# Optimization experiments

Hardware: AMD Instinct MI355X
Metric: run time of the kernel (lower is better)

Reference implementation:

```python
import jax, jax.numpy as jnp
import numpy as np

WIN = 7
SHIFT = 3
HEADS = 12
DIM = 384
HID = 4 * DIM
B, H, W = 32, 56, 56
N = WIN * WIN  # window area
EPS = 1e-5


def _rel_pos_index():
    coords = np.stack(np.meshgrid(np.arange(WIN), np.arange(WIN), indexing='ij'))  # (2,7,7)
    flat = coords.reshape(2, -1)  # (2,49)
    rel = flat[:, :, None] - flat[:, None, :]  # (2,49,49)
    rel = rel.transpose(1, 2, 0)
    rel[:, :, 0] += WIN - 1
    rel[:, :, 1] += WIN - 1
    rel[:, :, 0] *= 2 * WIN - 1
    return rel.sum(-1)  # (49,49) indices into (2*7-1)^2=169 table


def _attn_mask():
    img = np.zeros((H, W), dtype=np.float32)
    hs = [(0, H - WIN), (H - WIN, H - SHIFT), (H - SHIFT, H)]
    ws = [(0, W - WIN), (W - WIN, W - SHIFT), (W - SHIFT, W)]
    cnt = 0
    for h0, h1 in hs:
        for w0, w1 in ws:
            img[h0:h1, w0:w1] = cnt
            cnt += 1
    mw = img.reshape(H // WIN, WIN, W // WIN, WIN).transpose(0, 2, 1, 3).reshape(-1, N)  # (nW,49)
    d = mw[:, None, :] - mw[:, :, None]
    return np.where(d != 0, -100.0, 0.0).astype(np.float32)  # (nW,49,49)


_RPI = jnp.asarray(_rel_pos_index())
_MASK = jnp.asarray(_attn_mask())


def _ln(t, w, b):
    m = t.mean(-1, keepdims=True)
    v = ((t - m) ** 2).mean(-1, keepdims=True)
    return (t - m) * jax.lax.rsqrt(v + EPS) * w + b


def setup_inputs() -> dict:
    key = jax.random.key(0)
    ks = jax.random.split(key, 16)
    s = 0.02
    return {
        'x': jax.random.normal(ks[0], (B, H, W, DIM), jnp.float32),
        'norm1_w': jnp.ones((DIM,), jnp.float32),
        'norm1_b': jnp.zeros((DIM,), jnp.float32),
        'qkv_w': jax.random.normal(ks[1], (3 * DIM, DIM), jnp.float32) * s,
        'qkv_b': jnp.zeros((3 * DIM,), jnp.float32),
        'rel_bias_table': jax.random.normal(ks[2], ((2 * WIN - 1) ** 2, HEADS), jnp.float32) * s,
        'proj_w': jax.random.normal(ks[3], (DIM, DIM), jnp.float32) * s,
        'proj_b': jnp.zeros((DIM,), jnp.float32),
        'norm2_w': jnp.ones((DIM,), jnp.float32),
        'norm2_b': jnp.zeros((DIM,), jnp.float32),
        'fc1_w': jax.random.normal(ks[4], (HID, DIM), jnp.float32) * s,
        'fc1_b': jnp.zeros((HID,), jnp.float32),
        'fc2_w': jax.random.normal(ks[5], (DIM, HID), jnp.float32) * s,
        'fc2_b': jnp.zeros((DIM,), jnp.float32),
    }


def reference(x, norm1_w, norm1_b, qkv_w, qkv_b, rel_bias_table, proj_w, proj_b,
              norm2_w, norm2_b, fc1_w, fc1_b, fc2_w, fc2_b):
    Bt, Ht, Wt, C = x.shape
    hd = C // HEADS
    nh, nw = Ht // WIN, Wt // WIN
    nWtot = nh * nw

    # ---- attention branch ----
    h = _ln(x, norm1_w, norm1_b)
    h = jnp.roll(h, (-SHIFT, -SHIFT), axis=(1, 2))
    # window partition -> (B*nW, N, C)
    hw = h.reshape(Bt, nh, WIN, nw, WIN, C).transpose(0, 1, 3, 2, 4, 5).reshape(-1, N, C)
    qkv = hw @ qkv_w.T + qkv_b  # (B_, N, 3C)
    qkv = qkv.reshape(-1, N, 3, HEADS, hd).transpose(2, 0, 3, 1, 4)
    q, k, v = qkv[0], qkv[1], qkv[2]  # (B_, heads, N, hd)
    scale = hd ** -0.5
    attn = jnp.einsum('bhnd,bhmd->bhnm', q * scale, k)
    bias = rel_bias_table[_RPI].transpose(2, 0, 1)  # (heads, N, N)
    attn = attn + bias[None]
    attn = attn.reshape(Bt, nWtot, HEADS, N, N) + _MASK[None, :, None]
    attn = jax.nn.softmax(attn, axis=-1).reshape(-1, HEADS, N, N)
    o = jnp.einsum('bhnm,bhmd->bhnd', attn, v)
    o = o.transpose(0, 2, 1, 3).reshape(-1, N, C)
    o = o @ proj_w.T + proj_b
    # window reverse + roll back
    o = o.reshape(Bt, nh, nw, WIN, WIN, C).transpose(0, 1, 3, 2, 4, 5).reshape(Bt, Ht, Wt, C)
    o = jnp.roll(o, (SHIFT, SHIFT), axis=(1, 2))
    x = x + o

    # ---- MLP branch ----
    h = _ln(x, norm2_w, norm2_b)
    h = jax.nn.gelu(h @ fc1_w.T + fc1_b, approximate=False)
    h = h @ fc2_w.T + fc2_b
    return x + h
```

## Files before the change

### kernel.cpp

```cpp
#include <hip/hip_runtime.h>
#include <hip/hip_bf16.h>
#include <math.h>

using bf16 = __hip_bfloat16;
typedef short bf16x8 __attribute__((ext_vector_type(8)));
typedef float f32x4 __attribute__((ext_vector_type(4)));

static constexpr int  TOK     = 100352;
static constexpr long QKV_SEG = 38535168L;

__device__ __forceinline__ float bf2f(short u) {
    return __uint_as_float(((unsigned)(unsigned short)u) << 16);
}
__device__ __forceinline__ short f2bs(float x) {
    union { bf16 b; short s; } u; u.b = __float2bfloat16(x); return u.s;
}
__device__ __forceinline__ void gload16(const void* g, void* l) {
    __builtin_amdgcn_global_load_lds(
        (const __attribute__((address_space(1))) unsigned int*)g,
        (__attribute__((address_space(3))) unsigned int*)l, 16, 0, 0);
}
__device__ __forceinline__ float gelu_fast(float x) {
    const float x2 = x * x;
    const float t1 = x * x2;
    const float y  = fmaf(0.071354816222f, t1, 1.5957691216f * x);
    const float e  = __expf(-y);
    return x * __frcp_rn(1.f + e);
}

__global__ __launch_bounds__(256)
void convert_w_kernel(const float* __restrict__ qkv_w, const float* __restrict__ proj_w,
                      const float* __restrict__ fc1_w, const float* __restrict__ fc2_w,
                      bf16* __restrict__ out)
{
    const int i4 = (blockIdx.x * 256 + threadIdx.x) * 4;
    if (i4 >= 1769472) return;
    const float* src; int off;
    if (i4 < 442368)       { src = qkv_w;  off = i4; }
    else if (i4 < 589824)  { src = proj_w; off = i4 - 442368; }
    else if (i4 < 1179648) { src = fc1_w;  off = i4 - 589824; }
    else                   { src = fc2_w;  off = i4 - 1179648; }
    const float4 v = *(const float4*)&src[off];
    out[i4+0] = __float2bfloat16(v.x);
    out[i4+1] = __float2bfloat16(v.y);
    out[i4+2] = __float2bfloat16(v.z);
    out[i4+3] = __float2bfloat16(v.w);
}

template<bool WINDOWED>
__global__ __launch_bounds__(256)
void ln_kernel(const float* __restrict__ x, const float* __restrict__ gw,
               const float* __restrict__ gb, bf16* __restrict__ out)
{
    const int wave = threadIdx.x >> 6;
    const int lane = threadIdx.x & 63;
    const long t = (long)blockIdx.x * 4 + wave;
    size_t src;
    if (WINDOWED) {
        int bb = (int)(t / 3136); int rem = (int)(t - (long)bb * 3136);
        int wIdx = rem / 49;      int n = rem - wIdx * 49;
        int wh = wIdx >> 3, ww = wIdx & 7;
        int yi = n / 7,     xi = n - yi * 7;
        int r = wh * 7 + yi + 3; if (r >= 56) r -= 56;
        int c = ww * 7 + xi + 3; if (c >= 56) c -= 56;
        src = ((size_t)bb * 3136 + (size_t)r * 56 + c) * 384;
    } else {
        src = (size_t)t * 384;
    }
    float v[6]; float s = 0.f, sq = 0.f;
    #pragma unroll
    for (int kk = 0; kk < 6; ++kk) {
        v[kk] = x[src + lane + 64 * kk];
        s += v[kk]; sq += v[kk] * v[kk];
    }
    #pragma unroll
    for (int o = 32; o > 0; o >>= 1) { s += __shfl_xor(s, o); sq += __shfl_xor(sq, o); }
    const float m   = s * (1.f / 384.f);
    const float var = sq * (1.f / 384.f) - m * m;
    const float rs  = rsqrtf(var + 1e-5f);
    #pragma unroll
    for (int kk = 0; kk < 6; ++kk) {
        int ch = lane + 64 * kk;
        out[(size_t)t * 384 + ch] = __float2bfloat16((v[kk] - m) * rs * gw[ch] + gb[ch]);
    }
}

template<int MODE>
__global__ __launch_bounds__(256)
void gemm_bt(const bf16* __restrict__ A, const bf16* __restrict__ W,
             const float* __restrict__ bias, bf16* __restrict__ outb,
             float* __restrict__ outf, const float* __restrict__ resid,
             int K, int tilesN)
{
    __shared__ bf16 As[128 * 64];
    __shared__ bf16 Bs[128 * 64];
    const int nwg = gridDim.x;
    const int b0  = blockIdx.x;
    const int swz = (b0 & 7) * (nwg >> 3) + (b0 >> 3);
    const int tm = swz / tilesN;
    const int tn = swz - tm * tilesN;
    const int tid  = threadIdx.x;
    const int lane = tid & 63;
    const int wid  = tid >> 6;
    const int wr = (wid >> 1) * 64;
    const int wc = (wid & 1) * 64;
    const int sr = tid >> 3;
    const int sc = (tid & 7) * 8;

    f32x4 acc[4][4];
    #pragma unroll
    for (int i = 0; i < 4; ++i)
        #pragma unroll
        for (int j = 0; j < 4; ++j) acc[i][j] = (f32x4)0.0f;

    const long am0 = (long)tm * 128;
    const int  bn0 = tn * 128;

    for (int k0 = 0; k0 < K; k0 += 64) {
        #pragma unroll
        for (int p = 0; p < 4; ++p) {
            const int row = p * 32 + sr;
            gload16(&A[(size_t)(am0 + row) * K + k0 + sc], &As[row * 64 + sc]);
            gload16(&W[(size_t)(bn0 + row) * K + k0 + sc], &Bs[row * 64 + sc]);
        }
        __syncthreads();
        #pragma unroll
        for (int kk = 0; kk < 2; ++kk) {
            const int kof = kk * 32 + (lane >> 4) * 8;
            bf16x8 aF[4], bF[4];
            #pragma unroll
            for (int mi = 0; mi < 4; ++mi)
                aF[mi] = *(const bf16x8*)&As[(wr + mi * 16 + (lane & 15)) * 64 + kof];
            #pragma unroll
            for (int ni = 0; ni < 4; ++ni)
                bF[ni] = *(const bf16x8*)&Bs[(wc + ni * 16 + (lane & 15)) * 64 + kof];
            #pragma unroll
            for (int ni = 0; ni < 4; ++ni)
                #pragma unroll
                for (int mi = 0; mi < 4; ++mi)
                    acc[ni][mi] = __builtin_amdgcn_mfma_f32_16x16x32_bf16(
                        bF[ni], aF[mi], acc[ni][mi], 0, 0, 0);
        }
        __syncthreads();
    }

    #pragma unroll
    for (int nf = 0; nf < 4; ++nf) {
        const int gn0 = bn0 + wc + nf * 16 + ((lane >> 4) << 2);
        const float4 bv = *(const float4*)&bias[gn0];
        int s3 = 0, hh = 0, d0 = 0;
        if (MODE == 0) {
            s3 = gn0 / 384; const int rem = gn0 - s3 * 384;
            hh = rem >> 5; d0 = rem & 31;
        }
        #pragma unroll
        for (int mf = 0; mf < 4; ++mf) {
            const long gm = am0 + wr + mf * 16 + (lane & 15);
            float vals[4];
            #pragma unroll
            for (int r = 0; r < 4; ++r) vals[r] = acc[nf][mf][r] + ((const float*)&bv)[r];

            if (MODE == 0) {
                long wwi = gm / 49; int ntok = (int)(gm - wwi * 49);
                size_t dst = (size_t)s3 * QKV_SEG
                           + ((size_t)(wwi * 12 + hh) * 49 + ntok) * 32 + d0;
                union { short h4[4]; uint2 u2; } pk;
                if (s3 == 0) {
                    #pragma unroll
                    for (int r = 0; r < 4; ++r)
                        pk.h4[r] = f2bs(vals[r] * 0.17677669529663687f);
                } else {
                    #pragma unroll
                    for (int r = 0; r < 4; ++r) pk.h4[r] = f2bs(vals[r]);
                }
                *(uint2*)&outb[dst] = pk.u2;
            } else if (MODE == 1) {
                int bb = (int)(gm / 3136); int rem = (int)(gm - (long)bb * 3136);
                int wIdx = rem / 49; int n = rem - wIdx * 49;
                int wh = wIdx >> 3, ww2 = wIdx & 7;
                int yi = n / 7,     xi = n - yi * 7;
                int rr = wh * 7 + yi + 3; if (rr >= 56) rr -= 56;
                int cc = ww2 * 7 + xi + 3; if (cc >= 56) cc -= 56;
                size_t dst = ((size_t)bb * 3136 + (size_t)rr * 56 + cc) * 384 + gn0;
                const float4 rv = *(const float4*)&resid[dst];
                float4 ov;
                ov.x = rv.x + vals[0]; ov.y = rv.y + vals[1];
                ov.z = rv.z + vals[2]; ov.w = rv.w + vals[3];
                *(float4*)&outf[dst] = ov;
            } else if (MODE == 2) {
                union { short h4[4]; uint2 u2; } pk;
                #pragma unroll
                for (int r = 0; r < 4; ++r) pk.h4[r] = f2bs(gelu_fast(vals[r]));
                *(uint2*)&outb[(size_t)gm * 1536 + gn0] = pk.u2;
            } else {
                size_t dst = (size_t)gm * 384 + gn0;
                const float4 rv = *(const float4*)&resid[dst];
                float4 ov;
                ov.x = rv.x + vals[0]; ov.y = rv.y + vals[1];
                ov.z = rv.z + vals[2]; ov.w = rv.w + vals[3];
                *(float4*)&outf[dst] = ov;
            }
        }
    }
}

__global__ __launch_bounds__(256)
void attn_mfma(const bf16* __restrict__ q, const bf16* __restrict__ k,
               const bf16* __restrict__ v, const float* __restrict__ table,
               bf16* __restrict__ o)
{
    __shared__ bf16  vt_s[4][2048];
    __shared__ bf16  p_s[4][4096];
    __shared__ float tbl_s[4][169];

    const int tid  = threadIdx.x;
    const int wid  = tid >> 6;
    const int lane = tid & 63;
    const int li = lane & 15, g = lane >> 4;
    const int gwh = blockIdx.x * 4 + wid;
    const int w = gwh / 12, h = gwh - w * 12;
    const int wIdx = w & 63;
    const int bh = wIdx >> 3, bw = wIdx & 7;
    const size_t base = (size_t)gwh * 1568;

    char* vt = (char*)vt_s[wid];
    char* ps = (char*)p_s[wid];

    for (int t = lane; t < 169; t += 64) tbl_s[wid][t] = table[t * 12 + h];

    {
        const int4 z = {0, 0, 0, 0};
        #pragma unroll
        for (int t = 0; t < 4; ++t) ((int4*)vt)[t * 64 + lane] = z;
        for (int t = lane; t < 196; t += 64) {
            const int j = t >> 2, d0 = (t & 3) * 8;
            bf16x8 row = *(const bf16x8*)&v[base + (size_t)j * 32 + d0];
            #pragma unroll
            for (int u = 0; u < 8; ++u) {
                const int d = d0 + u;
                int off = (d << 7) + (j << 1);
                off ^= (d & 7) << 4;
                *(short*)(vt + off) = row[u];
            }
        }
    }

    bf16x8 aK[4], bQ[4];
    const int koff = g * 8;
    #pragma unroll
    for (int mj = 0; mj < 4; ++mj)
        aK[mj] = *(const bf16x8*)&k[base + (size_t)(mj * 16 + li) * 32 + koff];
    #pragma unroll
    for (int ni = 0; ni < 4; ++ni)
        bQ[ni] = *(const bf16x8*)&q[base + (size_t)(ni * 16 + li) * 32 + koff];

    f32x4 acc[4][4];
    #pragma unroll
    for (int i = 0; i < 4; ++i)
        #pragma unroll
        for (int j = 0; j < 4; ++j) acc[i][j] = (f32x4)0.0f;
    #pragma unroll
    for (int mj = 0; mj < 4; ++mj)
        #pragma unroll
        for (int ni = 0; ni < 4; ++ni)
            acc[mj][ni] = __builtin_amdgcn_mfma_f32_16x16x32_bf16(
                aK[mj], bQ[ni], acc[mj][ni], 0, 0, 0);

    const bool bndH = (bh == 7), bndW = (bw == 7);
    #pragma unroll
    for (int ni = 0; ni < 4; ++ni) {
        const int i = ni * 16 + li;
        const int yi = i / 7, xi = i - yi * 7;
        const int ri = (bndH ? (yi < 4 ? 3 : 6) : 0) + (bndW ? (xi < 4 ? 1 : 2) : 0);
        float mx = -1e30f;
        #pragma unroll
        for (int mj = 0; mj < 4; ++mj)
            #pragma unroll
            for (int r = 0; r < 4; ++r) {
                const int j = mj * 16 + g * 4 + r;
                const int yj = j / 7, xj = j - yj * 7;
                int ridx = (yi - yj + 6) * 13 + (xi - xj + 6);
                ridx = max(0, min(168, ridx));
                float val = acc[mj][ni][r] + tbl_s[wid][ridx];
                const int rj = (bndH ? (yj < 4 ? 3 : 6) : 0) + (bndW ? (xj < 4 ? 1 : 2) : 0);
                if (ri != rj) val -= 100.f;
                if (j >= 49) val = -1e30f;
                acc[mj][ni][r] = val;
                mx = fmaxf(mx, val);
            }
        mx = fmaxf(mx, __shfl_xor(mx, 16));
        mx = fmaxf(mx, __shfl_xor(mx, 32));
        float sum = 0.f;
        #pragma unroll
        for (int mj = 0; mj < 4; ++mj)
            #pragma unroll
            for (int r = 0; r < 4; ++r) {
                const float p = __expf(acc[mj][ni][r] - mx);
                acc[mj][ni][r] = p; sum += p;
            }
        sum += __shfl_xor(sum, 16);
        sum += __shfl_xor(sum, 32);
        const float inv = 1.f / sum;
        #pragma unroll
        for (int mj = 0; mj < 4; ++mj) {
            union { short h4[4]; uint2 u2; } pk;
            #pragma unroll
            for (int r = 0; r < 4; ++r) pk.h4[r] = f2bs(acc[mj][ni][r] * inv);
            int off = (i << 7) + ((mj * 16 + g * 4) << 1);
            off ^= (i & 7) << 4;
            *(uint2*)(ps + off) = pk.u2;
        }
    }

    f32x4 acc2[2][4];
    #pragma unroll
    for (int i = 0; i < 2; ++i)
        #pragma unroll
        for (int j = 0; j < 4; ++j) acc2[i][j] = (f32x4)0.0f;
    #pragma unroll
    for (int kk = 0; kk < 2; ++kk) {
        bf16x8 aV[2], bP[4];
        #pragma unroll
        for (int md = 0; md < 2; ++md) {
            const int d = md * 16 + li;
            int off = (d << 7) + kk * 64 + g * 16;
            off ^= (d & 7) << 4;
            aV[md] = *(const bf16x8*)(vt + off);
        }
        #pragma unroll
        for (int ni = 0; ni < 4; ++ni) {
            const int i = ni * 16 + li;
            int off = (i << 7) + kk * 64 + g * 16;
            off ^= (i & 7) << 4;
            bP[ni] = *(const bf16x8*)(ps + off);
        }
        #pragma unroll
        for (int md = 0; md < 2; ++md)
            #pragma unroll
            for (int ni = 0; ni < 4; ++ni)
                acc2[md][ni] = __builtin_amdgcn_mfma_f32_16x16x32_bf16(
                    aV[md], bP[ni], acc2[md][ni], 0, 0, 0);
    }

    const size_t obase = (size_t)w * 49 * 384 + h * 32;
    #pragma unroll
    for (int ni = 0; ni < 4; ++ni) {
        const int i = ni * 16 + li;
        if (i < 49) {
            #pragma unroll
            for (int md = 0; md < 2; ++md) {
                const int d0 = md * 16 + g * 4;
                union { short h4[4]; uint2 u2; } pk;
                #pragma unroll
                for (int r = 0; r < 4; ++r) pk.h4[r] = f2bs(acc2[md][ni][r]);
                *(uint2*)&o[obase + (size_t)i * 384 + d0] = pk.u2;
            }
        }
    }
}

extern "C" void kernel_launch(void* const* d_in, const int* in_sizes, int n_in,
                              void* d_out, int out_size, void* d_ws, size_t ws_size,
                              hipStream_t stream) {
    const float* x      = (const float*)d_in[0];
    const float* n1w    = (const float*)d_in[1];
    const float* n1b    = (const float*)d_in[2];
    const float* qkv_w  = (const float*)d_in[3];
    const float* qkv_b  = (const float*)d_in[4];
    const float* table  = (const float*)d_in[5];
    const float* proj_w = (const float*)d_in[6];
    const float* proj_b = (const float*)d_in[7];
    const float* n2w    = (const float*)d_in[8];
    const float* n2b    = (const float*)d_in[9];
    const float* fc1_w  = (const float*)d_in[10];
    const float* fc1_b  = (const float*)d_in[11];
    const float* fc2_w  = (const float*)d_in[12];
    const float* fc2_b  = (const float*)d_in[13];
    float* out = (float*)d_out;

    char* ws = (char*)d_ws;
    bf16* buf0 = (bf16*)ws;
    bf16* buf1 = (bf16*)(ws + 77070336);
    bf16* wb   = (bf16*)(ws + 77070336 + 308281344);

    convert_w_kernel<<<1728, 256, 0, stream>>>(qkv_w, proj_w, fc1_w, fc2_w, wb);
    ln_kernel<true><<<TOK / 4, 256, 0, stream>>>(x, n1w, n1b, buf0);
    gemm_bt<0><<<784 * 9, 256, 0, stream>>>(buf0, wb, qkv_b,
                                            buf1, nullptr, nullptr, 384, 9);
    attn_mfma<<<2048 * 12 / 4, 256, 0, stream>>>(buf1, buf1 + QKV_SEG,
                                                 buf1 + 2 * QKV_SEG, table, buf0);
    gemm_bt<1><<<784 * 3, 256, 0, stream>>>(buf0, wb + 442368, proj_b,
                                            nullptr, out, x, 384, 3);
    ln_kernel<false><<<TOK / 4, 256, 0, stream>>>(out, n2w, n2b, buf0);
    gemm_bt<2><<<784 * 12, 256, 0, stream>>>(buf0, wb + 589824, fc1_b,
                                             buf1, nullptr, nullptr, 384, 12);
    gemm_bt<3><<<784 * 3, 256, 0, stream>>>(buf1, wb + 1179648, fc2_b,
                                            nullptr, out, out, 1536, 3);
}
```

Before: 1.010 ms.

## Double-buffer GEMM LDS tiles and XOR-swizzle columns to avoid bank conflicts

The GEMM main loop now uses two LDS buffers per operand, issuing the async global-to-LDS loads for the next K tile before computing the current one, so memory latency overlaps MFMA work. Global source columns are XOR-permuted by row so the fragment reads from LDS land on different banks. This doubles LDS usage per block, which may lower occupancy.

New measurement: 962.9 us. 4.7% less time.

```diff
diff --git a/kernel.cpp b/kernel.cpp
--- a/kernel.cpp
+++ b/kernel.cpp
@@ -92,8 +92,8 @@
              float* __restrict__ outf, const float* __restrict__ resid,
              int K, int tilesN)
 {
-    __shared__ bf16 As[128 * 64];
-    __shared__ bf16 Bs[128 * 64];
+    __shared__ bf16 As[2][128 * 64];
+    __shared__ bf16 Bs[2][128 * 64];
     const int nwg = gridDim.x;
     const int b0  = blockIdx.x;
     const int swz = (b0 & 7) * (nwg >> 3) + (b0 >> 3);
@@ -106,6 +106,7 @@
     const int wc = (wid & 1) * 64;
     const int sr = tid >> 3;
     const int sc = (tid & 7) * 8;
+    const int scs = sc ^ ((sr & 7) << 3);
 
     f32x4 acc[4][4];
     #pragma unroll
@@ -115,34 +116,53 @@
 
     const long am0 = (long)tm * 128;
     const int  bn0 = tn * 128;
-
-    for (int k0 = 0; k0 < K; k0 += 64) {
-        #pragma unroll
-        for (int p = 0; p < 4; ++p) {
-            const int row = p * 32 + sr;
-            gload16(&A[(size_t)(am0 + row) * K + k0 + sc], &As[row * 64 + sc]);
-            gload16(&W[(size_t)(bn0 + row) * K + k0 + sc], &Bs[row * 64 + sc]);
-        }
+    const bf16* Ab = A + am0 * K + scs;
+    const bf16* Wb = W + (long)bn0 * K + scs;
+
+    #define STAGE(bufi, k0_) do {                                          \
+        _Pragma("unroll")                                                   \
+        for (int p = 0; p < 4; ++p) {                                       \
+            const int row_ = p * 32 + sr;                                   \
+            gload16(&Ab[(size_t)row_ * K + (k0_)], &As[bufi][row_ * 64 + sc]); \
+            gload16(&Wb[(size_t)row_ * K + (k0_)], &Bs[bufi][row_ * 64 + sc]); \
+        } } while (0)
+
+    const int rophase = (lane & 7) << 3;
+    const int kbase   = (lane >> 4) * 8;
+
+    #define COMPUTE(bufi) do {                                              \
+        _Pragma("unroll")                                                   \
+        for (int kk = 0; kk < 2; ++kk) {                                    \
+            const int kofs = (kk * 32 + kbase) ^ rophase;                   \
+            bf16x8 aF[4], bF[4];                                            \
+            _Pragma("unroll")                                               \
+            for (int mi = 0; mi < 4; ++mi)                                  \
+                aF[mi] = *(const bf16x8*)&As[bufi][(wr + mi * 16 + (lane & 15)) * 64 + kofs]; \
+            _Pragma("unroll")                                               \
+            for (int ni = 0; ni < 4; ++ni)                                  \
+                bF[ni] = *(const bf16x8*)&Bs[bufi][(wc + ni * 16 + (lane & 15)) * 64 + kofs]; \
+            _Pragma("unroll")                                               \
+            for (int ni = 0; ni < 4; ++ni)                                  \
+                _Pragma("unroll")                                           \
+                for (int mi = 0; mi < 4; ++mi)                              \
+                    acc[ni][mi] = __builtin_amdgcn_mfma_f32_16x16x32_bf16(  \
+                        bF[ni], aF[mi], acc[ni][mi], 0, 0, 0);              \
+        } } while (0)
+
+    STAGE(0, 0);
+    __syncthreads();
+    int cur = 0;
+    const int nsteps = K >> 6;
+    for (int t = 0; t < nsteps - 1; ++t) {
+        STAGE(cur ^ 1, (t + 1) << 6);
+        __builtin_amdgcn_sched_barrier(0);
+        COMPUTE(cur);
         __syncthreads();
-        #pragma unroll
-        for (int kk = 0; kk < 2; ++kk) {
-            const int kof = kk * 32 + (lane >> 4) * 8;
-            bf16x8 aF[4], bF[4];
-            #pragma unroll
-            for (int mi = 0; mi < 4; ++mi)
-                aF[mi] = *(const bf16x8*)&As[(wr + mi * 16 + (lane & 15)) * 64 + kof];
-            #pragma unroll
-            for (int ni = 0; ni < 4; ++ni)
-                bF[ni] = *(const bf16x8*)&Bs[(wc + ni * 16 + (lane & 15)) * 64 + kof];
-            #pragma unroll
-            for (int ni = 0; ni < 4; ++ni)
-                #pragma unroll
-                for (int mi = 0; mi < 4; ++mi)
-                    acc[ni][mi] = __builtin_amdgcn_mfma_f32_16x16x32_bf16(
-                        bF[ni], aF[mi], acc[ni][mi], 0, 0, 0);
-        }
-        __syncthreads();
-    }
+        cur ^= 1;
+    }
+    COMPUTE(cur);
+    #undef STAGE
+    #undef COMPUTE
 
     #pragma unroll
     for (int nf = 0; nf < 4; ++nf) {
```

## Swizzle GEMM LDS layout, hoist epilogue index math, raise occupancy hint

Applied to the files above, without the earlier changes.

Applies an XOR swizzle to the K offset of the global source address for the LDS staging loads, paired with a matching XOR on the fragment reads. Because global_load_lds writes each lane at a fixed LDS slot, the swizzle is applied on the global side, and the goal is fewer LDS bank conflicts on the MFMA fragment loads. The epilogue now loops over rows first, so the per-token divisions and window-reverse index math run once per row rather than once per column fragment. It also replaces the bf16 conversion with an inline round-to-nearest-even bit trick, which skips NaN handling, and adds a min-blocks-per-CU occupancy hint that may force register spills.

New measurement: 1.986 ms. +96.6%, slower.

```diff
diff --git a/kernel.cpp b/kernel.cpp
--- a/kernel.cpp
+++ b/kernel.cpp
@@ -13,7 +13,9 @@
     return __uint_as_float(((unsigned)(unsigned short)u) << 16);
 }
 __device__ __forceinline__ short f2bs(float x) {
-    union { bf16 b; short s; } u; u.b = __float2bfloat16(x); return u.s;
+    unsigned u = __float_as_uint(x);
+    u += 0x7FFF + ((u >> 16) & 1);
+    return (short)(u >> 16);
 }
 __device__ __forceinline__ void gload16(const void* g, void* l) {
     __builtin_amdgcn_global_load_lds(
@@ -86,7 +88,7 @@
 }
 
 template<int MODE>
-__global__ __launch_bounds__(256)
+__global__ __launch_bounds__(256, 5)
 void gemm_bt(const bf16* __restrict__ A, const bf16* __restrict__ W,
              const float* __restrict__ bias, bf16* __restrict__ outb,
              float* __restrict__ outf, const float* __restrict__ resid,
@@ -106,6 +108,7 @@
     const int wc = (wid & 1) * 64;
     const int sr = tid >> 3;
     const int sc = (tid & 7) * 8;
+    const int scs = sc ^ ((sr & 7) << 3);
 
     f32x4 acc[4][4];
     #pragma unroll
@@ -115,25 +118,30 @@
 
     const long am0 = (long)tm * 128;
     const int  bn0 = tn * 128;
+    const bf16* Ab = A + am0 * K + scs;
+    const bf16* Wb = W + (long)bn0 * K + scs;
+
+    const int rophase = (lane & 7) << 3;
+    const int kbase   = (lane >> 4) * 8;
 
     for (int k0 = 0; k0 < K; k0 += 64) {
         #pragma unroll
         for (int p = 0; p < 4; ++p) {
             const int row = p * 32 + sr;
-            gload16(&A[(size_t)(am0 + row) * K + k0 + sc], &As[row * 64 + sc]);
-            gload16(&W[(size_t)(bn0 + row) * K + k0 + sc], &Bs[row * 64 + sc]);
+            gload16(&Ab[(size_t)row * K + k0], &As[row * 64 + sc]);
+            gload16(&Wb[(size_t)row * K + k0], &Bs[row * 64 + sc]);
         }
         __syncthreads();
         #pragma unroll
         for (int kk = 0; kk < 2; ++kk) {
-            const int kof = kk * 32 + (lane >> 4) * 8;
+            const int kofs = (kk * 32 + kbase) ^ rophase;
             bf16x8 aF[4], bF[4];
             #pragma unroll
             for (int mi = 0; mi < 4; ++mi)
-                aF[mi] = *(const bf16x8*)&As[(wr + mi * 16 + (lane & 15)) * 64 + kof];
+                aF[mi] = *(const bf16x8*)&As[(wr + mi * 16 + (lane & 15)) * 64 + kofs];
             #pragma unroll
             for (int ni = 0; ni < 4; ++ni)
-                bF[ni] = *(const bf16x8*)&Bs[(wc + ni * 16 + (lane & 15)) * 64 + kof];
+                bF[ni] = *(const bf16x8*)&Bs[(wc + ni * 16 + (lane & 15)) * 64 + kofs];
             #pragma unroll
             for (int ni = 0; ni < 4; ++ni)
                 #pragma unroll
@@ -144,24 +152,41 @@
         __syncthreads();
     }
 
+    const int g4 = (lane >> 4) << 2;
+    int    gn0c[4];
+    float4 bvc[4];
     #pragma unroll
     for (int nf = 0; nf < 4; ++nf) {
-        const int gn0 = bn0 + wc + nf * 16 + ((lane >> 4) << 2);
-        const float4 bv = *(const float4*)&bias[gn0];
-        int s3 = 0, hh = 0, d0 = 0;
+        gn0c[nf] = bn0 + wc + nf * 16 + g4;
+        bvc[nf]  = *(const float4*)&bias[gn0c[nf]];
+    }
+
+    #pragma unroll
+    for (int mf = 0; mf < 4; ++mf) {
+        const long gm = am0 + wr + mf * 16 + (lane & 15);
+        size_t tokdst = 0;
+        long wwi = 0; int ntok = 0;
         if (MODE == 0) {
-            s3 = gn0 / 384; const int rem = gn0 - s3 * 384;
-            hh = rem >> 5; d0 = rem & 31;
-        }
-        #pragma unroll
-        for (int mf = 0; mf < 4; ++mf) {
-            const long gm = am0 + wr + mf * 16 + (lane & 15);
+            wwi = gm / 49; ntok = (int)(gm - wwi * 49);
+        } else if (MODE == 1) {
+            int bb = (int)(gm / 3136); int rem = (int)(gm - (long)bb * 3136);
+            int wIdx = rem / 49; int n = rem - wIdx * 49;
+            int wh = wIdx >> 3, ww2 = wIdx & 7;
+            int yi = n / 7,     xi = n - yi * 7;
+            int rr = wh * 7 + yi + 3; if (rr >= 56) rr -= 56;
+            int cc = ww2 * 7 + xi + 3; if (cc >= 56) cc -= 56;
+            tokdst = ((size_t)bb * 3136 + (size_t)rr * 56 + cc) * 384;
+        }
+        #pragma unroll
+        for (int nf = 0; nf < 4; ++nf) {
+            const int gn0 = gn0c[nf];
             float vals[4];
             #pragma unroll
-            for (int r = 0; r < 4; ++r) vals[r] = acc[nf][mf][r] + ((const float*)&bv)[r];
+            for (int r = 0; r < 4; ++r) vals[r] = acc[nf][mf][r] + ((const float*)&bvc[nf])[r];
 
             if (MODE == 0) {
-                long wwi = gm / 49; int ntok = (int)(gm - wwi * 49);
+                const int s3 = gn0 / 384; const int rem = gn0 - s3 * 384;
+                const int hh = rem >> 5, d0 = rem & 31;
                 size_t dst = (size_t)s3 * QKV_SEG
                            + ((size_t)(wwi * 12 + hh) * 49 + ntok) * 32 + d0;
                 union { short h4[4]; uint2 u2; } pk;
@@ -175,13 +200,7 @@
                 }
                 *(uint2*)&outb[dst] = pk.u2;
             } else if (MODE == 1) {
-                int bb = (int)(gm / 3136); int rem = (int)(gm - (long)bb * 3136);
-                int wIdx = rem / 49; int n = rem - wIdx * 49;
-                int wh = wIdx >> 3, ww2 = wIdx & 7;
-                int yi = n / 7,     xi = n - yi * 7;
-                int rr = wh * 7 + yi + 3; if (rr >= 56) rr -= 56;
-                int cc = ww2 * 7 + xi + 3; if (cc >= 56) cc -= 56;
-                size_t dst = ((size_t)bb * 3136 + (size_t)rr * 56 + cc) * 384 + gn0;
+                size_t dst = tokdst + gn0;
                 const float4 rv = *(const float4*)&resid[dst];
                 float4 ov;
                 ov.x = rv.x + vals[0]; ov.y = rv.y + vals[1];
```
